# Optimization experiments

Hardware: AMD Instinct MI355X
Metric: run time of the kernel (lower is better)

The kernel has to match this reference:

```python
import jax, jax.numpy as jnp
import numpy as np

HEADS = 4
DIM_HEAD = 32
GROUPS = 32  # min(256//4, 32)
EPS = 1e-5


def setup_inputs() -> dict:
    key = jax.random.key(0)
    ks = jax.random.split(key, 6)
    B, C, H, W = 16, 256, 64, 64
    hidden = HEADS * DIM_HEAD  # 128
    return {
        "x": jax.random.normal(ks[0], (B, C, H, W), dtype=jnp.float32),
        "gn_w": jax.random.uniform(ks[1], (C,), dtype=jnp.float32),
        "gn_b": jax.random.normal(ks[2], (C,), dtype=jnp.float32) * 0.05,
        "qkv_w": jax.random.normal(ks[3], (3 * hidden, C), dtype=jnp.float32) * 0.05,
        "qkv_b": jax.random.normal(ks[4], (3 * hidden,), dtype=jnp.float32) * 0.05,
        "out_w": jax.random.normal(ks[5], (C, hidden), dtype=jnp.float32) * 0.05,
        "out_b": jnp.zeros((C,), dtype=jnp.float32),
    }


def _forward_single(x, gn_w, gn_b, qkv_w, qkv_b, out_w, out_b):
    # x: (c, h, w)
    c, h, w = x.shape
    # GroupNorm over (channels-in-group, h, w)
    xg = x.reshape(GROUPS, c // GROUPS, h, w)
    mean = xg.mean(axis=(1, 2, 3), keepdims=True)
    var = xg.var(axis=(1, 2, 3), keepdims=True)
    xn = ((xg - mean) * jax.lax.rsqrt(var + EPS)).reshape(c, h, w)
    xn = xn * gn_w[:, None, None] + gn_b[:, None, None]
    # 1x1 conv QKV projection
    qkv = jnp.einsum('oc,chw->ohw', qkv_w, xn) + qkv_b[:, None, None]
    qkv = qkv.reshape(3, HEADS, DIM_HEAD, h * w)
    q, k, v = qkv[0], qkv[1], qkv[2]
    k = jax.nn.softmax(k, axis=-1)  # softmax over spatial
    context = jnp.einsum('hdn,hen->hde', k, v)   # (heads, d, d)
    out = jnp.einsum('hde,hdn->hen', context, q)  # (heads, d, n)
    out = out.reshape(HEADS * DIM_HEAD, h, w)
    # 1x1 conv output projection
    return jnp.einsum('oc,chw->ohw', out_w, out) + out_b[:, None, None]


def reference(x, gn_w, gn_b, qkv_w, qkv_b, out_w, out_b):
    f = lambda xi: _forward_single(xi, gn_w, gn_b, qkv_w, qkv_b, out_w, out_b)
    return jax.vmap(f)(x)
```

## Files before the change

### kernel.cpp

```cpp
#include <hip/hip_runtime.h>
#include <stdint.h>

typedef unsigned short u16;
typedef __attribute__((ext_vector_type(8))) short bf16x8;
typedef __attribute__((ext_vector_type(4))) float f32x4;

#define B_   16
#define C_   256
#define HW_  4096
#define QR_  384
#define HID_ 128

__device__ __forceinline__ float b2f(u16 u) {
  union { uint32_t i; float f; } v; v.i = ((uint32_t)u) << 16; return v.f;
}
__device__ __forceinline__ u16 f2b(float f) {
  union { float f; uint32_t i; } v; v.f = f;
  uint32_t r = (v.i + 0x7FFFu + ((v.i >> 16) & 1u)) >> 16;
  return (u16)r;
}

__global__ __launch_bounds__(256) void convw_kernel(
    const float* __restrict__ src, u16* __restrict__ dst, int n4)
{
  int i = blockIdx.x * 256 + threadIdx.x;
  if (i >= n4) return;
  float4 f = ((const float4*)src)[i];
  ushort4 o;
  o.x = f2b(f.x); o.y = f2b(f.y); o.z = f2b(f.z); o.w = f2b(f.w);
  ((ushort4*)dst)[i] = o;
}

__global__ __launch_bounds__(256) void gn_stats_kernel(
    const float* __restrict__ x, const float* __restrict__ gnw,
    const float* __restrict__ gnb, float* __restrict__ scale,
    float* __restrict__ shiftv)
{
  int b = blockIdx.x >> 5, g = blockIdx.x & 31;
  const float* p = x + ((size_t)b * C_ + g * 8) * HW_;
  int t = threadIdx.x;
  float s = 0.f, sq = 0.f;
#pragma unroll
  for (int i = 0; i < 16; ++i) {
    float4 u0 = *(const float4*)(p + t * 8 + i * 2048);
    float4 u1 = *(const float4*)(p + t * 8 + i * 2048 + 4);
    s  += u0.x + u0.y + u0.z + u0.w + u1.x + u1.y + u1.z + u1.w;
    sq += u0.x*u0.x + u0.y*u0.y + u0.z*u0.z + u0.w*u0.w
        + u1.x*u1.x + u1.y*u1.y + u1.z*u1.z + u1.w*u1.w;
  }
#pragma unroll
  for (int off = 32; off > 0; off >>= 1) {
    s  += __shfl_down(s, off);
    sq += __shfl_down(sq, off);
  }
  __shared__ float ps[4], pq[4], mr[2];
  int lane = t & 63, w = t >> 6;
  if (lane == 0) { ps[w] = s; pq[w] = sq; }
  __syncthreads();
  if (t == 0) {
    float S = ps[0] + ps[1] + ps[2] + ps[3];
    float Q = pq[0] + pq[1] + pq[2] + pq[3];
    float mean = S * (1.f / 32768.f);
    float var  = Q * (1.f / 32768.f) - mean * mean;
    mr[0] = mean; mr[1] = rsqrtf(var + 1e-5f);
  }
  __syncthreads();
  if (t < 8) {
    int c = g * 8 + t;
    float sc = gnw[c] * mr[1];
    scale[b * C_ + c]  = sc;
    shiftv[b * C_ + c] = gnb[c] - mr[0] * sc;
  }
}

__global__ __launch_bounds__(256) void gn_transpose_kernel(
    const float* __restrict__ x, u16* __restrict__ dst,
    const float* __restrict__ scale, const float* __restrict__ shiftv)
{
  int nt = blockIdx.x, ct = blockIdx.y, b = blockIdx.z;
  const float* S = x + (size_t)b * C_ * HW_;
  u16* D = dst + (size_t)b * HW_ * C_;
  __shared__ __align__(16) u16 tile[64][136];
  int t = threadIdx.x;
  int n0 = nt * 128, c0 = ct * 64;
  int r = t >> 2, seg = (t & 3) * 32;
  float sc = scale[(size_t)b * C_ + c0 + r];
  float sh = shiftv[(size_t)b * C_ + c0 + r];
#pragma unroll
  for (int i = 0; i < 4; ++i) {
    const float* rp = S + (size_t)(c0 + r) * HW_ + n0 + seg + i * 8;
    float4 u0 = *(const float4*)(rp);
    float4 u1 = *(const float4*)(rp + 4);
    float f[8] = {u0.x, u0.y, u0.z, u0.w, u1.x, u1.y, u1.z, u1.w};
    uint4 o;
    uint32_t* op = (uint32_t*)&o;
#pragma unroll
    for (int j = 0; j < 4; ++j) {
      op[j] = (uint32_t)f2b(f[2 * j] * sc + sh)
            | ((uint32_t)f2b(f[2 * j + 1] * sc + sh) << 16);
    }
    *(uint4*)&tile[r][seg + i * 8] = o;
  }
  __syncthreads();
#pragma unroll
  for (int i = 0; i < 4; ++i) {
    int m = t * 4 + i;
    int n_l = m >> 3, cg = (m & 7) * 8;
    union { u16 v[8]; uint4 q; } pk;
#pragma unroll
    for (int e = 0; e < 8; ++e) pk.v[e] = tile[cg + e][n_l];
    *(uint4*)(D + (size_t)(n0 + n_l) * C_ + c0 + cg) = pk.q;
  }
}

__global__ __launch_bounds__(256) void qkv_gemm_kernel(
    const u16* __restrict__ A, const u16* __restrict__ Bt,
    const float* __restrict__ bias, u16* __restrict__ qkv,
    u16* __restrict__ q_t)
{
  const int K = C_;
  int nt = blockIdx.x, mt = blockIdx.y, b = blockIdx.z;
  const u16* Ab = A + (size_t)mt * 128 * K;
  const u16* Bb = Bt + (size_t)b * HW_ * C_ + (size_t)nt * 128 * K;
  __shared__ __align__(16) u16 smem[128 * 136];
  u16* lA = smem;
  u16* lB = smem + 8192;
  int t = threadIdx.x;
  int lane = t & 63, w = t >> 6;
  int quad = lane >> 4, l16 = lane & 15;
  int wm = (w >> 1) * 64, wn = (w & 1) * 64;
  f32x4 acc[4][4];
#pragma unroll
  for (int i = 0; i < 4; ++i)
#pragma unroll
    for (int j = 0; j < 4; ++j)
#pragma unroll
      for (int r = 0; r < 4; ++r) acc[i][j][r] = 0.f;

  for (int k0 = 0; k0 < K; k0 += 64) {
    __syncthreads();
#pragma unroll
    for (int q = 0; q < 4; ++q) {
      int ch = q * 256 + t;
      int row = ch >> 3, off = (ch & 7) * 8;
      __builtin_amdgcn_global_load_lds(
          (const __attribute__((address_space(1))) void*)(Ab + (size_t)row * K + k0 + off),
          (__attribute__((address_space(3))) void*)(lA + ch * 8), 16, 0, 0);
      __builtin_amdgcn_global_load_lds(
          (const __attribute__((address_space(1))) void*)(Bb + (size_t)row * K + k0 + off),
          (__attribute__((address_space(3))) void*)(lB + ch * 8), 16, 0, 0);
    }
    __syncthreads();
    const bf16x8* A8 = (const bf16x8*)lA;
    const bf16x8* B8 = (const bf16x8*)lB;
#pragma unroll
    for (int kk = 0; kk < 2; ++kk) {
      bf16x8 af[4], bfr[4];
#pragma unroll
      for (int i = 0; i < 4; ++i) af[i]  = A8[(wm + i * 16 + l16) * 8 + kk * 4 + quad];
#pragma unroll
      for (int j = 0; j < 4; ++j) bfr[j] = B8[(wn + j * 16 + l16) * 8 + kk * 4 + quad];
#pragma unroll
      for (int i = 0; i < 4; ++i)
#pragma unroll
        for (int j = 0; j < 4; ++j)
          acc[i][j] = __builtin_amdgcn_mfma_f32_16x16x32_bf16(af[i], bfr[j],
                                                              acc[i][j], 0, 0, 0);
    }
  }

  if (mt == 0) {
    __syncthreads();
#pragma unroll
    for (int i = 0; i < 4; ++i) {
      int o0 = wm + i * 16 + quad * 4;
      float b0 = bias[o0], b1 = bias[o0 + 1], b2 = bias[o0 + 2], b3 = bias[o0 + 3];
#pragma unroll
      for (int j = 0; j < 4; ++j) {
        int n_l = wn + j * 16 + l16;
        uint2 pk;
        pk.x = (uint32_t)f2b(acc[i][j][0] + b0) | ((uint32_t)f2b(acc[i][j][1] + b1) << 16);
        pk.y = (uint32_t)f2b(acc[i][j][2] + b2) | ((uint32_t)f2b(acc[i][j][3] + b3) << 16);
        *(uint2*)&smem[n_l * 136 + o0] = pk;
      }
    }
    __syncthreads();
    int n_l = t >> 1, half = t & 1;
    u16* dst = q_t + (size_t)b * HW_ * HID_ + (size_t)(nt * 128 + n_l) * HID_ + half * 64;
    const u16* srcp = smem + n_l * 136 + half * 64;
#pragma unroll
    for (int i = 0; i < 8; ++i)
      *(uint4*)(dst + i * 8) = *(const uint4*)(srcp + i * 8);
  } else {
#pragma unroll
    for (int i = 0; i < 4; ++i) {
#pragma unroll
      for (int rg = 0; rg < 4; ++rg) {
        int o = mt * 128 + wm + i * 16 + quad * 4 + rg;
        float bsv = bias[o];
        size_t rowbase = (size_t)b * QR_ * HW_ + (size_t)o * HW_;
#pragma unroll
        for (int j = 0; j < 4; ++j) {
          int n = nt * 128 + wn + j * 16 + l16;
          qkv[rowbase + n] = f2b(acc[i][j][rg] + bsv);
        }
      }
    }
  }
}

__global__ __launch_bounds__(1024) void ctxwf_kernel(
    const u16* __restrict__ qkv, const float* __restrict__ outw,
    u16* __restrict__ wf)
{
  int b = blockIdx.x >> 2, h = blockIdx.x & 3;
  const u16* kb = qkv + ((size_t)b * QR_ + 128 + h * 32) * HW_;
  const u16* vb = qkv + ((size_t)b * QR_ + 256 + h * 32) * HW_;
  int t = threadIdx.x;
  int w = t >> 6, lane = t & 63;
  __shared__ float part[16][1024];
  __shared__ float cs[1024];
  __shared__ float mrow[32], srow[32];

  {
    int row = t >> 5, sub = t & 31;
    const u16* rp = kb + (size_t)row * HW_;
    float m = -3.0e38f, s = 0.f;
#pragma unroll
    for (int it = 0; it < 16; ++it) {
      bf16x8 v8 = *(const bf16x8*)(rp + sub * 8 + it * 256);
      const u16* e8 = (const u16*)&v8;
      float f[8];
#pragma unroll
      for (int e = 0; e < 8; ++e) f[e] = b2f(e8[e]);
      float lm = fmaxf(fmaxf(fmaxf(f[0], f[1]), fmaxf(f[2], f[3])),
                       fmaxf(fmaxf(f[4], f[5]), fmaxf(f[6], f[7])));
      float mn = fmaxf(m, lm);
      float ls = 0.f;
#pragma unroll
      for (int e = 0; e < 8; ++e) ls += __expf(f[e] - mn);
      s = s * __expf(m - mn) + ls;
      m = mn;
    }
#pragma unroll
    for (int off = 16; off > 0; off >>= 1) {
      float om = __shfl_down(m, off);
      float os = __shfl_down(s, off);
      float mn = fmaxf(m, om);
      s = s * __expf(m - mn) + os * __expf(om - mn);
      m = mn;
    }
    if ((lane & 31) == 0) { mrow[row] = m; srow[row] = s; }
  }
  __syncthreads();

  int quad = lane >> 4, l16 = lane & 15;
  float m0 = mrow[l16],      is0 = 1.f / srow[l16];
  float m1 = mrow[16 + l16], is1 = 1.f / srow[16 + l16];
  f32x4 acc[2][2];
#pragma unroll
  for (int i = 0; i < 2; ++i)
#pragma unroll
    for (int j = 0; j < 2; ++j)
#pragma unroll
      for (int r = 0; r < 4; ++r) acc[i][j][r] = 0.f;
  int kbase = w * 256;
  for (int it = 0; it < 8; ++it) {
    int n0 = kbase + it * 32 + quad * 8;
    bf16x8 k0 = *(const bf16x8*)(kb + (size_t)l16 * HW_ + n0);
    bf16x8 k1 = *(const bf16x8*)(kb + (size_t)(16 + l16) * HW_ + n0);
    bf16x8 v0 = *(const bf16x8*)(vb + (size_t)l16 * HW_ + n0);
    bf16x8 v1 = *(const bf16x8*)(vb + (size_t)(16 + l16) * HW_ + n0);
    bf16x8 a0, a1;
    const u16* k0p = (const u16*)&k0; u16* a0p = (u16*)&a0;
    const u16* k1p = (const u16*)&k1; u16* a1p = (u16*)&a1;
#pragma unroll
    for (int e = 0; e < 8; ++e) {
      a0p[e] = f2b(__expf(b2f(k0p[e]) - m0) * is0);
      a1p[e] = f2b(__expf(b2f(k1p[e]) - m1) * is1);
    }
    acc[0][0] = __builtin_amdgcn_mfma_f32_16x16x32_bf16(a0, v0, acc[0][0], 0, 0, 0);
    acc[0][1] = __builtin_amdgcn_mfma_f32_16x16x32_bf16(a0, v1, acc[0][1], 0, 0, 0);
    acc[1][0] = __builtin_amdgcn_mfma_f32_16x16x32_bf16(a1, v0, acc[1][0], 0, 0, 0);
    acc[1][1] = __builtin_amdgcn_mfma_f32_16x16x32_bf16(a1, v1, acc[1][1], 0, 0, 0);
  }
#pragma unroll
  for (int i = 0; i < 2; ++i)
#pragma unroll
    for (int j = 0; j < 2; ++j)
#pragma unroll
      for (int r = 0; r < 4; ++r) {
        int d = i * 16 + quad * 4 + r;
        int e = j * 16 + l16;
        part[w][d * 32 + e] = acc[i][j][r];
      }
  __syncthreads();
  {
    float a = 0.f;
#pragma unroll
    for (int ww = 0; ww < 16; ++ww) a += part[ww][t];
    cs[t] = a;
  }
  __syncthreads();

  int o = t & 255, dg = t >> 8;
  const float* wr = outw + (size_t)o * HID_ + h * 32;
  float wv[32];
#pragma unroll
  for (int e = 0; e < 32; ++e) wv[e] = wr[e];
  union { u16 v[8]; uint4 q; } pk;
#pragma unroll
  for (int dd = 0; dd < 8; ++dd) {
    int d = dg * 8 + dd;
    float a = 0.f;
#pragma unroll
    for (int e = 0; e < 32; ++e) a += wv[e] * cs[d * 32 + e];
    pk.v[dd] = f2b(a);
  }
  *(uint4*)(wf + ((size_t)b * C_ + o) * HID_ + h * 32 + dg * 8) = pk.q;
}

__global__ __launch_bounds__(256) void out_gemm_kernel(
    const u16* __restrict__ A, const u16* __restrict__ Bt,
    const float* __restrict__ bias, float* __restrict__ Cout)
{
  const int K = HID_;
  int nt = blockIdx.x, mt = blockIdx.y, b = blockIdx.z;
  const u16* Ab = A + (size_t)b * C_ * HID_ + (size_t)mt * 128 * K;
  const u16* Bb = Bt + (size_t)b * HW_ * HID_ + (size_t)nt * 128 * K;
  __shared__ __align__(16) u16 lA[128 * 64];
  __shared__ __align__(16) u16 lB[128 * 64];
  int t = threadIdx.x;
  int lane = t & 63, w = t >> 6;
  int quad = lane >> 4, l16 = lane & 15;
  int wm = (w >> 1) * 64, wn = (w & 1) * 64;
  f32x4 acc[4][4];
#pragma unroll
  for (int i = 0; i < 4; ++i)
#pragma unroll
    for (int j = 0; j < 4; ++j)
#pragma unroll
      for (int r = 0; r < 4; ++r) acc[i][j][r] = 0.f;

  for (int k0 = 0; k0 < K; k0 += 64) {
    __syncthreads();
#pragma unroll
    for (int q = 0; q < 4; ++q) {
      int ch = q * 256 + t;
      int row = ch >> 3, off = (ch & 7) * 8;
      __builtin_amdgcn_global_load_lds(
          (const __attribute__((address_space(1))) void*)(Ab + (size_t)row * K + k0 + off),
          (__attribute__((address_space(3))) void*)(lA + ch * 8), 16, 0, 0);
      __builtin_amdgcn_global_load_lds(
          (const __attribute__((address_space(1))) void*)(Bb + (size_t)row * K + k0 + off),
          (__attribute__((address_space(3))) void*)(lB + ch * 8), 16, 0, 0);
    }
    __syncthreads();
    const bf16x8* A8 = (const bf16x8*)lA;
    const bf16x8* B8 = (const bf16x8*)lB;
#pragma unroll
    for (int kk = 0; kk < 2; ++kk) {
      bf16x8 af[4], bfr[4];
#pragma unroll
      for (int i = 0; i < 4; ++i) af[i]  = A8[(wm + i * 16 + l16) * 8 + kk * 4 + quad];
#pragma unroll
      for (int j = 0; j < 4; ++j) bfr[j] = B8[(wn + j * 16 + l16) * 8 + kk * 4 + quad];
#pragma unroll
      for (int i = 0; i < 4; ++i)
#pragma unroll
        for (int j = 0; j < 4; ++j)
          acc[i][j] = __builtin_amdgcn_mfma_f32_16x16x32_bf16(af[i], bfr[j],
                                                              acc[i][j], 0, 0, 0);
    }
  }
#pragma unroll
  for (int i = 0; i < 4; ++i) {
#pragma unroll
    for (int rg = 0; rg < 4; ++rg) {
      int o = mt * 128 + wm + i * 16 + quad * 4 + rg;
      float bsv = bias[o];
      size_t rowbase = (size_t)b * C_ * HW_ + (size_t)o * HW_;
#pragma unroll
      for (int j = 0; j < 4; ++j) {
        int n = nt * 128 + wn + j * 16 + l16;
        Cout[rowbase + n] = acc[i][j][rg] + bsv;
      }
    }
  }
}

extern "C" void kernel_launch(void* const* d_in, const int* in_sizes, int n_in,
                              void* d_out, int out_size, void* d_ws, size_t ws_size,
                              hipStream_t stream)
{
  const float* x    = (const float*)d_in[0];
  const float* gnw  = (const float*)d_in[1];
  const float* gnb  = (const float*)d_in[2];
  const float* qkvw = (const float*)d_in[3];
  const float* qkvb = (const float*)d_in[4];
  const float* outw = (const float*)d_in[5];
  const float* outb = (const float*)d_in[6];

  char* p = (char*)d_ws;
  float* scale  = (float*)p;            p += (size_t)B_ * C_ * 4;
  float* shiftv = (float*)p;            p += (size_t)B_ * C_ * 4;
  u16* cqkvw = (u16*)p;                 p += (size_t)QR_ * C_ * 2;
  u16* xn_t  = (u16*)p;                 p += (size_t)B_ * HW_ * C_ * 2;
  u16* qkv   = (u16*)p;                 p += (size_t)B_ * QR_ * HW_ * 2;
  u16* q_t   = (u16*)p;                 p += (size_t)B_ * HW_ * HID_ * 2;
  u16* wf    = (u16*)p;

  convw_kernel<<<(QR_ * C_ / 4 + 255) / 256, 256, 0, stream>>>(qkvw, cqkvw, QR_ * C_ / 4);
  gn_stats_kernel<<<512, 256, 0, stream>>>(x, gnw, gnb, scale, shiftv);
  gn_transpose_kernel<<<dim3(32, 4, 16), 256, 0, stream>>>(x, xn_t, scale, shiftv);
  qkv_gemm_kernel<<<dim3(32, 3, 16), 256, 0, stream>>>(cqkvw, xn_t, qkvb, qkv, q_t);
  ctxwf_kernel<<<64, 1024, 0, stream>>>(qkv, outw, wf);
  out_gemm_kernel<<<dim3(32, 2, 16), 256, 0, stream>>>(wf, q_t, outb, (float*)d_out);
}
```

Measured before the change: 217.9 us.

## Defer softmax normalization in context kernel and fuse weight conversion into GN stats

Removes the separate max/sum pass over K in the context kernel: exp(k) is used unnormalized in the MFMA, row sums are accumulated alongside, and 1/sum is applied when forming the fused output weights. The bf16 weight conversion kernel is merged into the group-norm stats launch as extra blocks, saving one launch. Dropping the max subtraction risks exp overflow for large K values.

```diff
diff --git a/kernel.cpp b/kernel.cpp
--- a/kernel.cpp
+++ b/kernel.cpp
@@ -20,22 +20,20 @@
   return (u16)r;
 }
 
-__global__ __launch_bounds__(256) void convw_kernel(
-    const float* __restrict__ src, u16* __restrict__ dst, int n4)
-{
-  int i = blockIdx.x * 256 + threadIdx.x;
-  if (i >= n4) return;
-  float4 f = ((const float4*)src)[i];
-  ushort4 o;
-  o.x = f2b(f.x); o.y = f2b(f.y); o.z = f2b(f.z); o.w = f2b(f.w);
-  ((ushort4*)dst)[i] = o;
-}
-
-__global__ __launch_bounds__(256) void gn_stats_kernel(
+__global__ __launch_bounds__(256) void gn_stats_conv_kernel(
     const float* __restrict__ x, const float* __restrict__ gnw,
     const float* __restrict__ gnb, float* __restrict__ scale,
-    float* __restrict__ shiftv)
-{
+    float* __restrict__ shiftv,
+    const float* __restrict__ qkvw, u16* __restrict__ cqkvw)
+{
+  if (blockIdx.x >= 512) {
+    int i = (blockIdx.x - 512) * 256 + threadIdx.x;
+    float4 f = ((const float4*)qkvw)[i];
+    ushort4 o;
+    o.x = f2b(f.x); o.y = f2b(f.y); o.z = f2b(f.z); o.w = f2b(f.w);
+    ((ushort4*)cqkvw)[i] = o;
+    return;
+  }
   int b = blockIdx.x >> 5, g = blockIdx.x & 31;
   const float* p = x + ((size_t)b * C_ + g * 8) * HW_;
   int t = threadIdx.x;
@@ -218,45 +216,11 @@
   const u16* vb = qkv + ((size_t)b * QR_ + 256 + h * 32) * HW_;
   int t = threadIdx.x;
   int w = t >> 6, lane = t & 63;
+  int quad = lane >> 4, l16 = lane & 15;
   __shared__ float part[16][1024];
   __shared__ float cs[1024];
-  __shared__ float mrow[32], srow[32];
-
-  {
-    int row = t >> 5, sub = t & 31;
-    const u16* rp = kb + (size_t)row * HW_;
-    float m = -3.0e38f, s = 0.f;
-#pragma unroll
-    for (int it = 0; it < 16; ++it) {
-      bf16x8 v8 = *(const bf16x8*)(rp + sub * 8 + it * 256);
-      const u16* e8 = (const u16*)&v8;
-      float f[8];
-#pragma unroll
-      for (int e = 0; e < 8; ++e) f[e] = b2f(e8[e]);
-      float lm = fmaxf(fmaxf(fmaxf(f[0], f[1]), fmaxf(f[2], f[3])),
-                       fmaxf(fmaxf(f[4], f[5]), fmaxf(f[6], f[7])));
-      float mn = fmaxf(m, lm);
-      float ls = 0.f;
-#pragma unroll
-      for (int e = 0; e < 8; ++e) ls += __expf(f[e] - mn);
-      s = s * __expf(m - mn) + ls;
-      m = mn;
-    }
-#pragma unroll
-    for (int off = 16; off > 0; off >>= 1) {
-      float om = __shfl_down(m, off);
-      float os = __shfl_down(s, off);
-      float mn = fmaxf(m, om);
-      s = s * __expf(m - mn) + os * __expf(om - mn);
-      m = mn;
-    }
-    if ((lane & 31) == 0) { mrow[row] = m; srow[row] = s; }
-  }
-  __syncthreads();
-
-  int quad = lane >> 4, l16 = lane & 15;
-  float m0 = mrow[l16],      is0 = 1.f / srow[l16];
-  float m1 = mrow[16 + l16], is1 = 1.f / srow[16 + l16];
+  __shared__ float2 sred[1024];
+  __shared__ float sinv[32];
   f32x4 acc[2][2];
 #pragma unroll
   for (int i = 0; i < 2; ++i)
@@ -264,6 +228,7 @@
     for (int j = 0; j < 2; ++j)
 #pragma unroll
       for (int r = 0; r < 4; ++r) acc[i][j][r] = 0.f;
+  float s0 = 0.f, s1 = 0.f;
   int kbase = w * 256;
   for (int it = 0; it < 8; ++it) {
     int n0 = kbase + it * 32 + quad * 8;
@@ -276,8 +241,11 @@
     const u16* k1p = (const u16*)&k1; u16* a1p = (u16*)&a1;
 #pragma unroll
     for (int e = 0; e < 8; ++e) {
-      a0p[e] = f2b(__expf(b2f(k0p[e]) - m0) * is0);
-      a1p[e] = f2b(__expf(b2f(k1p[e]) - m1) * is1);
+      float e0 = __expf(b2f(k0p[e]));
+      float e1 = __expf(b2f(k1p[e]));
+      s0 += e0; s1 += e1;
+      a0p[e] = f2b(e0);
+      a1p[e] = f2b(e1);
     }
     acc[0][0] = __builtin_amdgcn_mfma_f32_16x16x32_bf16(a0, v0, acc[0][0], 0, 0, 0);
     acc[0][1] = __builtin_amdgcn_mfma_f32_16x16x32_bf16(a0, v1, acc[0][1], 0, 0, 0);
@@ -294,6 +262,7 @@
         int e = j * 16 + l16;
         part[w][d * 32 + e] = acc[i][j][r];
       }
+  sred[t] = make_float2(s0, s1);
   __syncthreads();
   {
     float a = 0.f;
@@ -301,6 +270,18 @@
     for (int ww = 0; ww < 16; ++ww) a += part[ww][t];
     cs[t] = a;
   }
+  if (t < 32) {
+    int d = t, lsel = d & 15;
+    float ssum = 0.f;
+#pragma unroll
+    for (int ww = 0; ww < 16; ++ww)
+#pragma unroll
+      for (int q = 0; q < 4; ++q) {
+        float2 v2 = sred[ww * 64 + q * 16 + lsel];
+        ssum += (d < 16) ? v2.x : v2.y;
+      }
+    sinv[d] = 1.f / ssum;
+  }
   __syncthreads();
 
   int o = t & 255, dg = t >> 8;
@@ -315,7 +296,7 @@
     float a = 0.f;
 #pragma unroll
     for (int e = 0; e < 32; ++e) a += wv[e] * cs[d * 32 + e];
-    pk.v[dd] = f2b(a);
+    pk.v[dd] = f2b(a * sinv[d]);
   }
   *(uint4*)(wf + ((size_t)b * C_ + o) * HID_ + h * 32 + dg * 8) = pk.q;
 }
@@ -410,8 +391,8 @@
   u16* q_t   = (u16*)p;                 p += (size_t)B_ * HW_ * HID_ * 2;
   u16* wf    = (u16*)p;
 
-  convw_kernel<<<(QR_ * C_ / 4 + 255) / 256, 256, 0, stream>>>(qkvw, cqkvw, QR_ * C_ / 4);
-  gn_stats_kernel<<<512, 256, 0, stream>>>(x, gnw, gnb, scale, shiftv);
+  gn_stats_conv_kernel<<<608, 256, 0, stream>>>(x, gnw, gnb, scale, shiftv,
+                                                qkvw, cqkvw);
   gn_transpose_kernel<<<dim3(32, 4, 16), 256, 0, stream>>>(x, xn_t, scale, shiftv);
   qkv_gemm_kernel<<<dim3(32, 3, 16), 256, 0, stream>>>(cqkvw, xn_t, qkvb, qkv, q_t);
   ctxwf_kernel<<<64, 1024, 0, stream>>>(qkv, outw, wf);
```

Result: faster. 205.8 us (-5.5%).
